# Performance work log

Hardware: AMD Instinct MI355X
Metric: run time of the kernel (lower is better)

The kernel has to match this reference:

```python
import jax, jax.numpy as jnp
import numpy as np

N = 100000   # nodes
E = 1600000  # edges
F = 128      # input/hidden dim
C = 3        # classes
G = 64       # graphs in batch


def setup_inputs() -> dict:
    key = jax.random.key(0)
    ks = jax.random.split(key, 12)
    s = 1.0 / np.sqrt(F)
    return {
        "x": jax.random.normal(ks[0], (N, F), dtype=jnp.float32),
        "edge_index": jax.random.randint(ks[1], (2, E), 0, N, dtype=jnp.int64),
        "batch": jnp.sort(jax.random.randint(ks[2], (N,), 0, G, dtype=jnp.int64)),
        "W1": jax.random.normal(ks[3], (F, F), dtype=jnp.float32) * s,
        "b1": jnp.zeros((F,), dtype=jnp.float32),
        "W2": jax.random.normal(ks[4], (F, F), dtype=jnp.float32) * s,
        "b2": jnp.zeros((F,), dtype=jnp.float32),
        "W3": jax.random.normal(ks[5], (F, F), dtype=jnp.float32) * s,
        "b3": jnp.zeros((F,), dtype=jnp.float32),
        "Wc": jax.random.normal(ks[6], (F, C), dtype=jnp.float32) * s,
        "bc": jnp.zeros((C,), dtype=jnp.float32),
    }


def reference(x, edge_index, batch, W1, b1, W2, b2, W3, b3, Wc, bc):
    n = x.shape[0]
    src, dst = edge_index[0], edge_index[1]
    # GCN adds self-loops: A_hat = A + I
    loops = jnp.arange(n, dtype=src.dtype)
    src_a = jnp.concatenate([src, loops])
    dst_a = jnp.concatenate([dst, loops])
    # symmetric normalization D^-1/2 (A+I) D^-1/2 (in-degree incl. self-loop)
    deg = jax.ops.segment_sum(jnp.ones_like(dst_a, dtype=x.dtype), dst_a, num_segments=n)
    dis = jnp.where(deg > 0, jax.lax.rsqrt(deg), 0.0)
    norm = dis[src_a] * dis[dst_a]  # [E+N]

    def gcn_conv(h, W, b):
        h = h @ W                                    # [N, F']
        msg = h[src_a] * norm[:, None]               # gather + scale
        agg = jax.ops.segment_sum(msg, dst_a, num_segments=n)  # scatter-add
        return agg + b

    h = jax.nn.relu(gcn_conv(x, W1, b1))   # dropout = identity in eval mode
    h = jax.nn.relu(gcn_conv(h, W2, b2))
    h = jax.nn.relu(gcn_conv(h, W3, b3))

    # global_mean_pool over graph ids
    sums = jax.ops.segment_sum(h, batch, num_segments=G)
    cnt = jax.ops.segment_sum(jnp.ones((n,), dtype=h.dtype), batch, num_segments=G)
    pooled = sums / jnp.maximum(cnt, 1.0)[:, None]
    return pooled @ Wc + bc
```

## Files before the change

### kernel.cpp

```cpp
#include <hip/hip_runtime.h>
#include <cstdint>
#include <cstddef>

#define FDIM 128
#define CHUNK 4096
#define BSHIFT 8
#define BMASK 255
#define MAXB 512

typedef unsigned short ushort_t;
typedef __attribute__((ext_vector_type(8))) short short8;
typedef __attribute__((ext_vector_type(4))) float floatx4;

__device__ inline ushort_t f2bf(float f) {
  unsigned u = __float_as_uint(f);
  u += 0x7fffu + ((u >> 16) & 1u);
  return (ushort_t)(u >> 16);
}
__device__ inline float bf2f(ushort_t h) {
  return __uint_as_float((unsigned)h << 16);
}


__global__ __launch_bounds__(256) void k_hist(const int* __restrict__ dst, int e,
                                              int nb, int* __restrict__ chunkHist) {
  __shared__ int h[MAXB];
  int c = blockIdx.x;
  int base = c * CHUNK;
  int end = min(base + CHUNK, e);
  for (int i = threadIdx.x; i < nb; i += 256) h[i] = 0;
  __syncthreads();
  for (int i = base + threadIdx.x; i < end; i += 256)
    atomicAdd(&h[dst[i] >> BSHIFT], 1);
  __syncthreads();
  for (int b = threadIdx.x; b < nb; b += 256)
    chunkHist[(size_t)c * nb + b] = h[b];
}

__global__ __launch_bounds__(512) void k_scan1(const int* __restrict__ chunkHist,
                                               int nchunks, int nb,
                                               int* __restrict__ chunkOff,
                                               int* __restrict__ bucketTotal) {
  __shared__ int sb[512];
  int b = blockIdx.x;
  int t = threadIdx.x;
  int base = 0;
  for (int c0 = 0; c0 < nchunks; c0 += 512) {
    int c = c0 + t;
    int v = (c < nchunks) ? chunkHist[(size_t)c * nb + b] : 0;
    int x = v;
    sb[t] = x;
    __syncthreads();
    for (int off = 1; off < 512; off <<= 1) {
      int y = (t >= off) ? sb[t - off] : 0;
      __syncthreads();
      x += y;
      sb[t] = x;
      __syncthreads();
    }
    if (c < nchunks) chunkOff[(size_t)c * nb + b] = base + x - v;
    int tileTot = sb[511];
    __syncthreads();
    base += tileTot;
  }
  if (t == 0) bucketTotal[b] = base;
}

__global__ __launch_bounds__(512) void k_scan2(const int* __restrict__ bucketTotal,
                                               int nb, int e,
                                               int* __restrict__ bucketBase) {
  __shared__ int sb[512];
  int t = threadIdx.x;
  int v = (t < nb) ? bucketTotal[t] : 0;
  int x = v;
  sb[t] = x;
  __syncthreads();
  for (int off = 1; off < 512; off <<= 1) {
    int y = (t >= off) ? sb[t - off] : 0;
    __syncthreads();
    x += y;
    sb[t] = x;
    __syncthreads();
  }
  if (t < nb) bucketBase[t] = x - v;
  if (t == 0) bucketBase[nb] = e;
}

__global__ __launch_bounds__(256) void k_bin(const int* __restrict__ src,
                                             const int* __restrict__ dst, int e, int nb,
                                             const int* __restrict__ chunkHist,
                                             const int* __restrict__ chunkOff,
                                             const int* __restrict__ bucketBase,
                                             unsigned* __restrict__ binned) {
  __shared__ unsigned sortedL[CHUNK];
  __shared__ int gtarget[CHUNK];
  __shared__ int lbase[MAXB], lcur[MAXB], gbase[MAXB];
  __shared__ int stmp[256];
  int c = blockIdx.x;
  int base = c * CHUNK;
  int end = min(base + CHUNK, e);
  for (int i = threadIdx.x; i < nb; i += 256) {
    lbase[i] = chunkHist[(size_t)c * nb + i];
    gbase[i] = bucketBase[i] + chunkOff[(size_t)c * nb + i];
  }
  __syncthreads();
  int carry = 0;
  for (int i0 = 0; i0 < nb; i0 += 256) {
    int i = i0 + threadIdx.x;
    int v = (i < nb) ? lbase[i] : 0;
    int x = v;
    stmp[threadIdx.x] = x;
    __syncthreads();
    for (int off = 1; off < 256; off <<= 1) {
      int y = (threadIdx.x >= off) ? stmp[threadIdx.x - off] : 0;
      __syncthreads();
      x += y;
      stmp[threadIdx.x] = x;
      __syncthreads();
    }
    if (i < nb) lbase[i] = carry + x - v;
    int tileTot = stmp[255];
    __syncthreads();
    carry += tileTot;
  }
  for (int i = threadIdx.x; i < nb; i += 256) lcur[i] = lbase[i];
  __syncthreads();
  for (int i = base + threadIdx.x; i < end; i += 256) {
    int d = dst[i];
    int sv = src[i];
    int b = d >> BSHIFT;
    int slot = atomicAdd(&lcur[b], 1);
    sortedL[slot] = ((unsigned)sv << BSHIFT) | (unsigned)(d & BMASK);
    gtarget[slot] = gbase[b] + (slot - lbase[b]);
  }
  __syncthreads();
  for (int i = threadIdx.x; i < end - base; i += 256)
    binned[gtarget[i]] = sortedL[i];
}

__global__ __launch_bounds__(256) void k_fill2(const unsigned* __restrict__ binned,
                                               const int* __restrict__ bucketBase, int n,
                                               int* __restrict__ rowStart,
                                               int* __restrict__ deg,
                                               float* __restrict__ dis,
                                               int* __restrict__ colIdx) {
  __shared__ int h[256], sb[256], cur[256];
  int b = blockIdx.x;
  int s0 = bucketBase[b], s1 = bucketBase[b + 1];
  int nodeBase = b << BSHIFT;
  int t = threadIdx.x;
  h[t] = 0;
  __syncthreads();
  for (int i = s0 + t; i < s1; i += 256) atomicAdd(&h[binned[i] & BMASK], 1);
  __syncthreads();
  int v = h[t];
  int x = v;
  sb[t] = x;
  __syncthreads();
  for (int off = 1; off < 256; off <<= 1) {
    int y = (t >= off) ? sb[t - off] : 0;
    __syncthreads();
    x += y;
    sb[t] = x;
    __syncthreads();
  }
  int start = s0 + x - v;
  cur[t] = start;
  int node = nodeBase + t;
  if (node < n) {
    rowStart[node] = start;
    deg[node] = v;
    dis[node] = rsqrtf((float)(v + 1));
  }
  __syncthreads();
  for (int i = s0 + t; i < s1; i += 256) {
    unsigned en = binned[i];
    int slot = atomicAdd(&cur[en & BMASK], 1);
    colIdx[slot] = (int)(en >> BSHIFT);
  }
}

__global__ __launch_bounds__(256) void k_prepw(const float* __restrict__ W1,
                                               const float* __restrict__ W2,
                                               const float* __restrict__ W3,
                                               ushort_t* __restrict__ out) {
  int b = blockIdx.x;
  const float* W = (b == 0) ? W1 : (b == 1) ? W2 : W3;
  ushort_t* o = out + (size_t)b * 16384;
  for (int idx = threadIdx.x; idx < 16384; idx += 256) {
    int j = idx & 7;
    int lane = (idx >> 3) & 63;
    int ct = (idx >> 9) & 7;
    int kc = idx >> 12;
    int k = kc * 32 + (lane >> 4) * 8 + j;
    int col = ct * 16 + (lane & 15);
    o[idx] = f2bf(W[k * FDIM + col]);
  }
}

template <int INBF>
__global__ __launch_bounds__(256) void k_mm(const void* __restrict__ Ain,
                                            const ushort_t* __restrict__ Wsw,
                                            ushort_t* __restrict__ O, int n) {
  __shared__ ushort_t Bs[16384];
  int tid = threadIdx.x;
  for (int q = tid; q < 2048; q += 256)
    ((uint4*)Bs)[q] = ((const uint4*)Wsw)[q];
  __syncthreads();

  int w = tid >> 6;
  int lane = tid & 63;
  int quad = lane >> 4;
  int l15 = lane & 15;
  int rb = blockIdx.x * 128 + w * 32;
  const float* Af = (const float*)Ain;
  const ushort_t* Ab = (const ushort_t*)Ain;

  int row0 = rb + l15;
  int row1 = rb + 16 + l15;
  bool v0 = row0 < n, v1 = row1 < n;

  floatx4 acc[2][8];
#pragma unroll
  for (int rt = 0; rt < 2; ++rt)
#pragma unroll
    for (int ct = 0; ct < 8; ++ct) acc[rt][ct] = floatx4{0.f, 0.f, 0.f, 0.f};

#pragma unroll
  for (int kc = 0; kc < 4; ++kc) {
    int k0 = kc * 32 + quad * 8;
    short8 a0 = short8{0, 0, 0, 0, 0, 0, 0, 0};
    short8 a1 = short8{0, 0, 0, 0, 0, 0, 0, 0};
    if (INBF) {
      if (v0) a0 = *(const short8*)&Ab[(size_t)row0 * FDIM + k0];
      if (v1) a1 = *(const short8*)&Ab[(size_t)row1 * FDIM + k0];
    } else {
      if (v0) {
        float4 f0 = *(const float4*)&Af[(size_t)row0 * FDIM + k0];
        float4 f1 = *(const float4*)&Af[(size_t)row0 * FDIM + k0 + 4];
        a0 = short8{(short)f2bf(f0.x), (short)f2bf(f0.y), (short)f2bf(f0.z),
                    (short)f2bf(f0.w), (short)f2bf(f1.x), (short)f2bf(f1.y),
                    (short)f2bf(f1.z), (short)f2bf(f1.w)};
      }
      if (v1) {
        float4 f0 = *(const float4*)&Af[(size_t)row1 * FDIM + k0];
        float4 f1 = *(const float4*)&Af[(size_t)row1 * FDIM + k0 + 4];
        a1 = short8{(short)f2bf(f0.x), (short)f2bf(f0.y), (short)f2bf(f0.z),
                    (short)f2bf(f0.w), (short)f2bf(f1.x), (short)f2bf(f1.y),
                    (short)f2bf(f1.z), (short)f2bf(f1.w)};
      }
    }
#pragma unroll
    for (int ct = 0; ct < 8; ++ct) {
      short8 bf = *(const short8*)&Bs[((kc * 8 + ct) * 64 + lane) * 8];
      acc[0][ct] = __builtin_amdgcn_mfma_f32_16x16x32_bf16(a0, bf, acc[0][ct], 0, 0, 0);
      acc[1][ct] = __builtin_amdgcn_mfma_f32_16x16x32_bf16(a1, bf, acc[1][ct], 0, 0, 0);
    }
  }

#pragma unroll
  for (int rt = 0; rt < 2; ++rt) {
#pragma unroll
    for (int i = 0; i < 4; ++i) {
      int row = rb + rt * 16 + quad * 4 + i;
      if (row < n) {
#pragma unroll
        for (int ct = 0; ct < 8; ++ct)
          O[(size_t)row * FDIM + ct * 16 + l15] = f2bf(acc[rt][ct][i]);
      }
    }
  }
}

__global__ __launch_bounds__(256) void k_agg(const ushort_t* __restrict__ Hin,
                                             ushort_t* __restrict__ Hout,
                                             const int* __restrict__ rowStart,
                                             const int* __restrict__ degE,
                                             const int* __restrict__ colIdx,
                                             const float* __restrict__ dis,
                                             const float* __restrict__ bias, int n) {
  int node = blockIdx.x * 4 + (threadIdx.x >> 6);
  int lane = threadIdx.x & 63;
  if (node >= n) return;
  const unsigned* hin = (const unsigned*)Hin;
  float di = dis[node];
  unsigned us = hin[(size_t)node * 64 + lane];
  float ws = di * di;
  float ax = ws * __uint_as_float(us << 16);
  float ay = ws * __uint_as_float(us & 0xffff0000u);
  int s0 = rowStart[node], cnt = degE[node];
#pragma unroll 4
  for (int j = 0; j < cnt; ++j) {
    int s = colIdx[s0 + j];
    float w = di * dis[s];
    unsigned u = hin[(size_t)s * 64 + lane];
    ax += w * __uint_as_float(u << 16);
    ay += w * __uint_as_float(u & 0xffff0000u);
  }
  float2 b = ((const float2*)bias)[lane];
  ax = fmaxf(ax + b.x, 0.f);
  ay = fmaxf(ay + b.y, 0.f);
  unsigned out = (unsigned)f2bf(ax) | ((unsigned)f2bf(ay) << 16);
  ((unsigned*)Hout)[(size_t)node * 64 + lane] = out;
}


__global__ __launch_bounds__(128) void k_gstart(const int* __restrict__ batch, int n,
                                                int g_count, int* __restrict__ gstart) {
  int g = threadIdx.x;
  if (g > g_count) return;
  int lo = 0, hi = n;
  while (lo < hi) {
    int mid = (lo + hi) >> 1;
    if (batch[mid] < g) lo = mid + 1;
    else hi = mid;
  }
  gstart[g] = lo;
}

__global__ __launch_bounds__(128) void k_pool(const ushort_t* __restrict__ H,
                                              const int* __restrict__ gstart,
                                              float* __restrict__ pooled, int g_count) {
  int g = blockIdx.x >> 4;
  int c = blockIdx.x & 15;
  int s = gstart[g], e = gstart[g + 1];
  int len = e - s;
  int chunk = (len + 15) >> 4;
  int ns = s + c * chunk;
  int ne = min(ns + chunk, e);
  float acc = 0.f;
  for (int i = ns; i < ne; ++i) acc += bf2f(H[(size_t)i * FDIM + threadIdx.x]);
  atomicAdd(&pooled[g * FDIM + threadIdx.x], acc);
}

__global__ __launch_bounds__(192) void k_final(const float* __restrict__ pooled,
                                               const int* __restrict__ gstart,
                                               const float* __restrict__ Wc,
                                               const float* __restrict__ bc,
                                               float* __restrict__ out, int g_count) {
  int t = threadIdx.x;
  if (t >= g_count * 3) return;
  int g = t / 3, c = t % 3;
  int cnt = gstart[g + 1] - gstart[g];
  float inv = 1.0f / (float)max(cnt, 1);
  float acc = bc[c];
#pragma unroll 8
  for (int k = 0; k < FDIM; ++k) acc += pooled[g * FDIM + k] * inv * Wc[k * 3 + c];
  out[g * 3 + c] = acc;
}


extern "C" void kernel_launch(void* const* d_in, const int* in_sizes, int n_in,
                              void* d_out, int out_size, void* d_ws, size_t ws_size,
                              hipStream_t stream) {
  const float* x = (const float*)d_in[0];
  const int* edge = (const int*)d_in[1];
  const int* batch = (const int*)d_in[2];
  const float* W1 = (const float*)d_in[3];
  const float* b1 = (const float*)d_in[4];
  const float* W2 = (const float*)d_in[5];
  const float* b2 = (const float*)d_in[6];
  const float* W3 = (const float*)d_in[7];
  const float* b3 = (const float*)d_in[8];
  const float* Wc = (const float*)d_in[9];
  const float* bc = (const float*)d_in[10];
  float* out = (float*)d_out;

  const int N = in_sizes[0] / FDIM;
  const int E = in_sizes[1] / 2;
  const int G = out_size / 3;
  const int* src = edge;
  const int* dst = edge + E;

  const int NCH = (E + CHUNK - 1) / CHUNK;
  const int NB = (N + (1 << BSHIFT) - 1) >> BSHIFT;

  char* ws = (char*)d_ws;
  size_t off = 0;
  auto carve = [&](size_t bytes) -> void* {
    void* p = ws + off;
    off = (off + bytes + 255) & ~(size_t)255;
    return p;
  };
  ushort_t* h0 = (ushort_t*)carve((size_t)N * FDIM * 2);
  ushort_t* h1 = (ushort_t*)carve((size_t)N * FDIM * 2);
  int* colIdx = (int*)carve((size_t)E * 4);
  unsigned* binned = (unsigned*)carve((size_t)E * 4);
  int* chunkHist = (int*)carve((size_t)NCH * NB * 4);
  int* chunkOff = (int*)carve((size_t)NCH * NB * 4);
  int* bucketTotal = (int*)carve((size_t)NB * 4);
  int* bucketBase = (int*)carve((size_t)(NB + 1) * 4);
  int* rowStart = (int*)carve((size_t)N * 4);
  int* deg = (int*)carve((size_t)N * 4);
  float* dis = (float*)carve((size_t)N * 4);
  int* gstart = (int*)carve((size_t)(G + 1) * 4);
  float* pooled = (float*)carve((size_t)G * FDIM * 4);
  ushort_t* wsw = (ushort_t*)carve((size_t)3 * 16384 * 2);
  (void)n_in;
  (void)ws_size;

  hipMemsetAsync(pooled, 0, (size_t)G * FDIM * 4, stream);

  k_hist<<<NCH, 256, 0, stream>>>(dst, E, NB, chunkHist);
  k_scan1<<<NB, 512, 0, stream>>>(chunkHist, NCH, NB, chunkOff, bucketTotal);
  k_scan2<<<1, 512, 0, stream>>>(bucketTotal, NB, E, bucketBase);
  k_bin<<<NCH, 256, 0, stream>>>(src, dst, E, NB, chunkHist, chunkOff, bucketBase,
                                 binned);
  k_fill2<<<NB, 256, 0, stream>>>(binned, bucketBase, N, rowStart, deg, dis, colIdx);
  k_prepw<<<3, 256, 0, stream>>>(W1, W2, W3, wsw);

  int mmb = (N + 127) / 128;
  k_mm<0><<<mmb, 256, 0, stream>>>(x, wsw, h0, N);
  k_agg<<<(N + 3) / 4, 256, 0, stream>>>(h0, h1, rowStart, deg, colIdx, dis, b1, N);
  k_mm<1><<<mmb, 256, 0, stream>>>(h1, wsw + 16384, h0, N);
  k_agg<<<(N + 3) / 4, 256, 0, stream>>>(h0, h1, rowStart, deg, colIdx, dis, b2, N);
  k_mm<1><<<mmb, 256, 0, stream>>>(h1, wsw + 32768, h0, N);
  k_agg<<<(N + 3) / 4, 256, 0, stream>>>(h0, h1, rowStart, deg, colIdx, dis, b3, N);

  k_gstart<<<1, 128, 0, stream>>>(batch, N, G, gstart);
  k_pool<<<G * 16, 128, 0, stream>>>(h1, gstart, pooled, G);
  k_final<<<1, 192, 0, stream>>>(pooled, gstart, Wc, bc, out, G);
}
```

Baseline: 493.6 us.

## Store hidden features in feature-sliced layout and split aggregation across slices

Hidden activations are now stored as 8 slices of 16 bf16 features per node, with the GEMM, aggregation and pooling kernels indexing that layout. Aggregation launches one block group per slice. Within a wave, 8 edge groups process neighbours in parallel and combine their partial sums with shuffle reductions. The aim is a smaller per-slice gather working set for better cache locality and more edge-level parallelism. The cost is that each node's edge list and degree-normalisation values are now read once per slice, 8 times in total, and 32-byte gathers are less efficient.

```diff
diff --git a/kernel.cpp b/kernel.cpp
--- a/kernel.cpp
+++ b/kernel.cpp
@@ -3,6 +3,8 @@
 #include <cstddef>
 
 #define FDIM 128
+#define SLICES 8
+#define SW 16
 #define CHUNK 4096
 #define BSHIFT 8
 #define BMASK 255
@@ -232,8 +234,9 @@
     short8 a0 = short8{0, 0, 0, 0, 0, 0, 0, 0};
     short8 a1 = short8{0, 0, 0, 0, 0, 0, 0, 0};
     if (INBF) {
-      if (v0) a0 = *(const short8*)&Ab[(size_t)row0 * FDIM + k0];
-      if (v1) a1 = *(const short8*)&Ab[(size_t)row1 * FDIM + k0];
+      int sl = k0 >> 4, of = k0 & 15;
+      if (v0) a0 = *(const short8*)&Ab[((size_t)sl * n + row0) * SW + of];
+      if (v1) a1 = *(const short8*)&Ab[((size_t)sl * n + row1) * SW + of];
     } else {
       if (v0) {
         float4 f0 = *(const float4*)&Af[(size_t)row0 * FDIM + k0];
@@ -266,7 +269,7 @@
       if (row < n) {
 #pragma unroll
         for (int ct = 0; ct < 8; ++ct)
-          O[(size_t)row * FDIM + ct * 16 + l15] = f2bf(acc[rt][ct][i]);
+          O[((size_t)ct * n + row) * SW + l15] = f2bf(acc[rt][ct][i]);
       }
     }
   }
@@ -279,29 +282,45 @@
                                              const int* __restrict__ colIdx,
                                              const float* __restrict__ dis,
                                              const float* __restrict__ bias, int n) {
-  int node = blockIdx.x * 4 + (threadIdx.x >> 6);
+  int slice = blockIdx.x & 7;
+  int g = blockIdx.x >> 3;
+  int wave = threadIdx.x >> 6;
   int lane = threadIdx.x & 63;
-  if (node >= n) return;
-  const unsigned* hin = (const unsigned*)Hin;
-  float di = dis[node];
-  unsigned us = hin[(size_t)node * 64 + lane];
-  float ws = di * di;
-  float ax = ws * __uint_as_float(us << 16);
-  float ay = ws * __uint_as_float(us & 0xffff0000u);
-  int s0 = rowStart[node], cnt = degE[node];
-#pragma unroll 4
-  for (int j = 0; j < cnt; ++j) {
-    int s = colIdx[s0 + j];
-    float w = di * dis[s];
-    unsigned u = hin[(size_t)s * 64 + lane];
-    ax += w * __uint_as_float(u << 16);
-    ay += w * __uint_as_float(u & 0xffff0000u);
-  }
-  float2 b = ((const float2*)bias)[lane];
-  ax = fmaxf(ax + b.x, 0.f);
-  ay = fmaxf(ay + b.y, 0.f);
-  unsigned out = (unsigned)f2bf(ax) | ((unsigned)f2bf(ay) << 16);
-  ((unsigned*)Hout)[(size_t)node * 64 + lane] = out;
+  int eg = lane >> 3;
+  int f = lane & 7;
+  const unsigned* hin = (const unsigned*)Hin + (size_t)slice * n * 8;
+  unsigned* hout = (unsigned*)Hout + (size_t)slice * n * 8;
+  float2 bv = ((const float2*)bias)[slice * 8 + f];
+
+  int node0 = (g * 4 + wave) * 8;
+  for (int ni = 0; ni < 8; ++ni) {
+    int node = node0 + ni;
+    if (node >= n) return;
+    float di = dis[node];
+    int s0 = rowStart[node], cnt = degE[node];
+    unsigned us = hin[(size_t)node * 8 + f];
+    float ws = (eg == 0) ? di * di : 0.f;
+    float ax = ws * __uint_as_float(us << 16);
+    float ay = ws * __uint_as_float(us & 0xffff0000u);
+    for (int j = eg; j < cnt; j += 8) {
+      int s = colIdx[s0 + j];
+      float w = di * dis[s];
+      unsigned u = hin[(size_t)s * 8 + f];
+      ax += w * __uint_as_float(u << 16);
+      ay += w * __uint_as_float(u & 0xffff0000u);
+    }
+    ax += __shfl_xor(ax, 8);
+    ay += __shfl_xor(ay, 8);
+    ax += __shfl_xor(ax, 16);
+    ay += __shfl_xor(ay, 16);
+    ax += __shfl_xor(ax, 32);
+    ay += __shfl_xor(ay, 32);
+    if (eg == 0) {
+      ax = fmaxf(ax + bv.x, 0.f);
+      ay = fmaxf(ay + bv.y, 0.f);
+      hout[(size_t)node * 8 + f] = (unsigned)f2bf(ax) | ((unsigned)f2bf(ay) << 16);
+    }
+  }
 }
 
 
@@ -320,16 +339,20 @@
 
 __global__ __launch_bounds__(128) void k_pool(const ushort_t* __restrict__ H,
                                               const int* __restrict__ gstart,
-                                              float* __restrict__ pooled, int g_count) {
+                                              float* __restrict__ pooled, int g_count,
+                                              int n) {
   int g = blockIdx.x >> 4;
   int c = blockIdx.x & 15;
+  int sl = threadIdx.x >> 4;
+  int of = threadIdx.x & 15;
   int s = gstart[g], e = gstart[g + 1];
   int len = e - s;
   int chunk = (len + 15) >> 4;
   int ns = s + c * chunk;
   int ne = min(ns + chunk, e);
   float acc = 0.f;
-  for (int i = ns; i < ne; ++i) acc += bf2f(H[(size_t)i * FDIM + threadIdx.x]);
+  for (int i = ns; i < ne; ++i)
+    acc += bf2f(H[((size_t)sl * n + i) * SW + of]);
   atomicAdd(&pooled[g * FDIM + threadIdx.x], acc);
 }
 
@@ -410,14 +433,15 @@
   k_prepw<<<3, 256, 0, stream>>>(W1, W2, W3, wsw);
 
   int mmb = (N + 127) / 128;
+  int aggb = ((N + 31) / 32) * 8;
   k_mm<0><<<mmb, 256, 0, stream>>>(x, wsw, h0, N);
-  k_agg<<<(N + 3) / 4, 256, 0, stream>>>(h0, h1, rowStart, deg, colIdx, dis, b1, N);
+  k_agg<<<aggb, 256, 0, stream>>>(h0, h1, rowStart, deg, colIdx, dis, b1, N);
   k_mm<1><<<mmb, 256, 0, stream>>>(h1, wsw + 16384, h0, N);
-  k_agg<<<(N + 3) / 4, 256, 0, stream>>>(h0, h1, rowStart, deg, colIdx, dis, b2, N);
+  k_agg<<<aggb, 256, 0, stream>>>(h0, h1, rowStart, deg, colIdx, dis, b2, N);
   k_mm<1><<<mmb, 256, 0, stream>>>(h1, wsw + 32768, h0, N);
-  k_agg<<<(N + 3) / 4, 256, 0, stream>>>(h0, h1, rowStart, deg, colIdx, dis, b3, N);
+  k_agg<<<aggb, 256, 0, stream>>>(h0, h1, rowStart, deg, colIdx, dis, b3, N);
 
   k_gstart<<<1, 128, 0, stream>>>(batch, N, G, gstart);
-  k_pool<<<G * 16, 128, 0, stream>>>(h1, gstart, pooled, G);
+  k_pool<<<G * 16, 128, 0, stream>>>(h1, gstart, pooled, G, N);
   k_final<<<1, 192, 0, stream>>>(pooled, gstart, Wc, bc, out, G);
 }
```

Result: slower. 914.7 us (+85.3%).

## Pack neighbor index with source norm and use half-wave 8-byte gathers in aggregation

Applied to the files above, without the earlier changes.

Adds a pass that stores each edge's source dis value next to its column index as an int2, so aggregation no longer does a dependent gather of dis[s] per edge. The aggregation kernel now assigns 32 lanes per node with 8-byte (4 bf16) loads instead of 64 lanes with 4-byte loads, processing 8 nodes per block. This cuts per-edge dependent load latency and instruction count and widens memory transactions. In exchange it doubles the size of the index array and adds one extra edge-wide kernel launch.

```diff
diff --git a/kernel.cpp b/kernel.cpp
--- a/kernel.cpp
+++ b/kernel.cpp
@@ -143,7 +143,7 @@
                                                int* __restrict__ rowStart,
                                                int* __restrict__ deg,
                                                float* __restrict__ dis,
-                                               int* __restrict__ colIdx) {
+                                               int2* __restrict__ colPair) {
   __shared__ int h[256], sb[256], cur[256];
   int b = blockIdx.x;
   int s0 = bucketBase[b], s1 = bucketBase[b + 1];
@@ -176,7 +176,17 @@
   for (int i = s0 + t; i < s1; i += 256) {
     unsigned en = binned[i];
     int slot = atomicAdd(&cur[en & BMASK], 1);
-    colIdx[slot] = (int)(en >> BSHIFT);
+    colPair[slot] = int2{(int)(en >> BSHIFT), 0};
+  }
+}
+
+__global__ __launch_bounds__(256) void k_edgew(int2* __restrict__ colPair, int e,
+                                               const float* __restrict__ dis) {
+  int i = blockIdx.x * 256 + threadIdx.x;
+  if (i < e) {
+    int2 p = colPair[i];
+    p.y = __float_as_int(dis[p.x]);
+    colPair[i] = p;
   }
 }
 
@@ -276,32 +286,40 @@
                                              ushort_t* __restrict__ Hout,
                                              const int* __restrict__ rowStart,
                                              const int* __restrict__ degE,
-                                             const int* __restrict__ colIdx,
+                                             const int2* __restrict__ colPair,
                                              const float* __restrict__ dis,
                                              const float* __restrict__ bias, int n) {
-  int node = blockIdx.x * 4 + (threadIdx.x >> 6);
-  int lane = threadIdx.x & 63;
+  int node = blockIdx.x * 8 + (threadIdx.x >> 5);
+  int lane = threadIdx.x & 31;
   if (node >= n) return;
-  const unsigned* hin = (const unsigned*)Hin;
+  const uint2* hin = (const uint2*)Hin;
   float di = dis[node];
-  unsigned us = hin[(size_t)node * 64 + lane];
+  uint2 su = hin[(size_t)node * 32 + lane];
   float ws = di * di;
-  float ax = ws * __uint_as_float(us << 16);
-  float ay = ws * __uint_as_float(us & 0xffff0000u);
+  float a0 = ws * __uint_as_float(su.x << 16);
+  float a1 = ws * __uint_as_float(su.x & 0xffff0000u);
+  float a2 = ws * __uint_as_float(su.y << 16);
+  float a3 = ws * __uint_as_float(su.y & 0xffff0000u);
   int s0 = rowStart[node], cnt = degE[node];
 #pragma unroll 4
   for (int j = 0; j < cnt; ++j) {
-    int s = colIdx[s0 + j];
-    float w = di * dis[s];
-    unsigned u = hin[(size_t)s * 64 + lane];
-    ax += w * __uint_as_float(u << 16);
-    ay += w * __uint_as_float(u & 0xffff0000u);
-  }
-  float2 b = ((const float2*)bias)[lane];
-  ax = fmaxf(ax + b.x, 0.f);
-  ay = fmaxf(ay + b.y, 0.f);
-  unsigned out = (unsigned)f2bf(ax) | ((unsigned)f2bf(ay) << 16);
-  ((unsigned*)Hout)[(size_t)node * 64 + lane] = out;
+    int2 p = colPair[s0 + j];
+    float w = di * __int_as_float(p.y);
+    uint2 u = hin[(size_t)p.x * 32 + lane];
+    a0 += w * __uint_as_float(u.x << 16);
+    a1 += w * __uint_as_float(u.x & 0xffff0000u);
+    a2 += w * __uint_as_float(u.y << 16);
+    a3 += w * __uint_as_float(u.y & 0xffff0000u);
+  }
+  float4 b = ((const float4*)bias)[lane];
+  a0 = fmaxf(a0 + b.x, 0.f);
+  a1 = fmaxf(a1 + b.y, 0.f);
+  a2 = fmaxf(a2 + b.z, 0.f);
+  a3 = fmaxf(a3 + b.w, 0.f);
+  uint2 o;
+  o.x = (unsigned)f2bf(a0) | ((unsigned)f2bf(a1) << 16);
+  o.y = (unsigned)f2bf(a2) | ((unsigned)f2bf(a3) << 16);
+  ((uint2*)Hout)[(size_t)node * 32 + lane] = o;
 }
 
 
@@ -384,7 +402,7 @@
   };
   ushort_t* h0 = (ushort_t*)carve((size_t)N * FDIM * 2);
   ushort_t* h1 = (ushort_t*)carve((size_t)N * FDIM * 2);
-  int* colIdx = (int*)carve((size_t)E * 4);
+  int2* colPair = (int2*)carve((size_t)E * 8);
   unsigned* binned = (unsigned*)carve((size_t)E * 4);
   int* chunkHist = (int*)carve((size_t)NCH * NB * 4);
   int* chunkOff = (int*)carve((size_t)NCH * NB * 4);
@@ -406,16 +424,18 @@
   k_scan2<<<1, 512, 0, stream>>>(bucketTotal, NB, E, bucketBase);
   k_bin<<<NCH, 256, 0, stream>>>(src, dst, E, NB, chunkHist, chunkOff, bucketBase,
                                  binned);
-  k_fill2<<<NB, 256, 0, stream>>>(binned, bucketBase, N, rowStart, deg, dis, colIdx);
+  k_fill2<<<NB, 256, 0, stream>>>(binned, bucketBase, N, rowStart, deg, dis, colPair);
+  k_edgew<<<(E + 255) / 256, 256, 0, stream>>>(colPair, E, dis);
   k_prepw<<<3, 256, 0, stream>>>(W1, W2, W3, wsw);
 
   int mmb = (N + 127) / 128;
+  int aggb = (N + 7) / 8;
   k_mm<0><<<mmb, 256, 0, stream>>>(x, wsw, h0, N);
-  k_agg<<<(N + 3) / 4, 256, 0, stream>>>(h0, h1, rowStart, deg, colIdx, dis, b1, N);
+  k_agg<<<aggb, 256, 0, stream>>>(h0, h1, rowStart, deg, colPair, dis, b1, N);
   k_mm<1><<<mmb, 256, 0, stream>>>(h1, wsw + 16384, h0, N);
-  k_agg<<<(N + 3) / 4, 256, 0, stream>>>(h0, h1, rowStart, deg, colIdx, dis, b2, N);
+  k_agg<<<aggb, 256, 0, stream>>>(h0, h1, rowStart, deg, colPair, dis, b2, N);
   k_mm<1><<<mmb, 256, 0, stream>>>(h1, wsw + 32768, h0, N);
-  k_agg<<<(N + 3) / 4, 256, 0, stream>>>(h0, h1, rowStart, deg, colIdx, dis, b3, N);
+  k_agg<<<aggb, 256, 0, stream>>>(h0, h1, rowStart, deg, colPair, dis, b3, N);
 
   k_gstart<<<1, 128, 0, stream>>>(batch, N, G, gstart);
   k_pool<<<G * 16, 128, 0, stream>>>(h1, gstart, pooled, G);
```

After: 453.5 us. 1.09x faster.
